# Performance work log

Hardware: AMD Instinct MI355X
Metric: run time of the kernel (lower is better)

## Reference

```python
import jax, jax.numpy as jnp
import numpy as np

N = 50000        # bs * n_node
E = 800000       # n_edge
INPUT_NF = 64
HIDDEN_NF = 64
N_CHANNEL = 4
D = 3            # spatial dim
EDGE_D = 16
EPS = 1e-12      # F.normalize clamp


def _unif(k, shape, fan_in):
    s = 1.0 / np.sqrt(fan_in)
    return jax.random.uniform(k, shape, jnp.float32, -s, s)


def setup_inputs() -> dict:
    key = jax.random.key(0)
    ks = jax.random.split(key, 12)
    h = jax.random.normal(ks[0], (N, INPUT_NF), jnp.float32)
    coord = jax.random.normal(ks[1], (N, N_CHANNEL, D), jnp.float32)
    row = jax.random.randint(ks[2], (E,), 0, N)
    col = jax.random.randint(ks[3], (E,), 0, N)
    edge_attr = jax.random.normal(ks[4], (E, EDGE_D), jnp.float32)
    kv_in = INPUT_NF + N_CHANNEL * N_CHANNEL + EDGE_D
    Wq = _unif(ks[5], (INPUT_NF, HIDDEN_NF), INPUT_NF)
    bq = _unif(ks[6], (HIDDEN_NF,), INPUT_NF)
    Wkv = _unif(ks[7], (kv_in, 2 * HIDDEN_NF), kv_in)
    bkv = _unif(ks[8], (2 * HIDDEN_NF,), kv_in)
    W1 = _unif(ks[9], (HIDDEN_NF, HIDDEN_NF), HIDDEN_NF)
    b1 = _unif(ks[10], (HIDDEN_NF,), HIDDEN_NF)
    # xavier_uniform with gain=0.001, no bias
    lim = 0.001 * np.sqrt(6.0 / (HIDDEN_NF + N_CHANNEL))
    W2 = jax.random.uniform(ks[11], (HIDDEN_NF, N_CHANNEL), jnp.float32, -lim, lim)
    return dict(h=h, coord=coord, row=row, col=col, edge_attr=edge_attr,
                Wq=Wq, bq=bq, Wkv=Wkv, bkv=bkv, W1=W1, b1=b1, W2=W2)


def reference(h, coord, edge_attr, Wq, bq, Wkv, bkv, W1, b1, W2, row, col):
    n_node = h.shape[0]
    # coord2radial
    coord_diff = coord[row] - coord[col]                                # [E,C,D]
    radial = jnp.einsum('ecd,efd->ecf', coord_diff, coord_diff)         # [E,C,C]
    # F.normalize(radial, dim=0): L2-normalize across the edge dimension
    norm = jnp.maximum(jnp.sqrt(jnp.sum(radial * radial, axis=0, keepdims=True)), EPS)
    radial = radial / norm
    # att_model
    q = h[row] @ Wq + bq                                                # [E,H]
    target_feat = jnp.concatenate(
        [radial.reshape(radial.shape[0], -1), h[col], edge_attr], axis=1)
    kv = target_feat @ Wkv + bkv                                        # [E,2H]
    k, v = kv[:, 0::2], kv[:, 1::2]                                     # [E,H] each
    alpha = jnp.sum(q * k, axis=1)                                      # [E]
    # scatter_softmax over segments given by row (numerically stable)
    seg_max = jax.ops.segment_max(alpha, row, num_segments=n_node)
    ex = jnp.exp(alpha - seg_max[row])
    seg_sum = jax.ops.segment_sum(ex, row, num_segments=n_node)
    att = ex / seg_sum[row]                                             # [E]
    # node_model (dropout in eval mode = identity)
    h_out = h + jax.ops.segment_sum(att[:, None] * v, row, num_segments=n_node)
    # coord_model: coord_mlp = Linear -> SiLU -> Linear(no bias)
    coord_v = att[:, None] * (jax.nn.silu(v @ W1 + b1) @ W2)            # [E,C]
    trans = coord_diff * coord_v[:, :, None]                            # [E,C,D]
    coord_out = coord + jax.ops.segment_sum(trans, row, num_segments=n_node)
    return h_out, coord_out, att
```

## Files before the change

kernel.cpp:

```cpp
#include <hip/hip_runtime.h>
#include <math.h>

#define NN 50000
#define NE 800000
#define NPREB 1024

typedef __attribute__((ext_vector_type(8))) short short8;
typedef __attribute__((ext_vector_type(4))) float floatx4;

__device__ __forceinline__ unsigned short bf16_of(float x) {
  unsigned u = __float_as_uint(x);
  u += 0x7fffu + ((u >> 16) & 1u);
  return (unsigned short)(u >> 16);
}
__device__ __forceinline__ float bf2f(unsigned short u) {
  return __uint_as_float(((unsigned)u) << 16);
}
__device__ __forceinline__ unsigned pack_bf(float a, float b) {
  unsigned ua = __float_as_uint(a); ua += 0x7fffu + ((ua >> 16) & 1u);
  unsigned ub = __float_as_uint(b); ub += 0x7fffu + ((ub >> 16) & 1u);
  return (ua >> 16) | (ub & 0xffff0000u);
}
__device__ __forceinline__ float blo(unsigned w) { return __uint_as_float(w << 16); }
__device__ __forceinline__ float bhi(unsigned w) { return __uint_as_float(w & 0xffff0000u); }

__global__ __launch_bounds__(256)
void k_pre(const float* __restrict__ coord, const int* __restrict__ row,
           const int* __restrict__ col, const float* __restrict__ Wkv,
           const float* __restrict__ W1, const float* __restrict__ Wq,
           float* __restrict__ norm_part, int* __restrict__ deg,
           unsigned short* __restrict__ Bkvb, unsigned short* __restrict__ W1tb,
           unsigned short* __restrict__ Wqtb) {
  __shared__ float nred[4][16];
  const int gid = blockIdx.x * 256 + threadIdx.x;
  const int np = gridDim.x * 256;
  for (int idx = gid; idx < 128 * 96; idx += np) {
    int n = idx & 127, kk = idx >> 7;
    float w = (n < 64) ? Wkv[kk * 128 + 2 * n] : Wkv[kk * 128 + 2 * (n - 64) + 1];
    Bkvb[n * 104 + kk] = bf16_of(w);
  }
  for (int idx = gid; idx < 64 * 64; idx += np) {
    int n = idx & 63, kk = idx >> 6;
    W1tb[n * 88 + kk] = bf16_of(W1[kk * 64 + n]);
  }
  for (int idx = gid; idx < 64 * 64; idx += np) {
    int n = idx & 63, kk = idx >> 6;
    Wqtb[n * 64 + kk] = bf16_of(Wq[kk * 64 + n]);
  }
  float accv[16];
#pragma unroll
  for (int j = 0; j < 16; ++j) accv[j] = 0.f;
  for (int e = gid; e < NE; e += np) {
    int r = row[e], c = col[e];
    const float4* cr = (const float4*)(coord + (size_t)r * 12);
    const float4* cc = (const float4*)(coord + (size_t)c * 12);
    float cd[12];
#pragma unroll
    for (int q = 0; q < 3; ++q) {
      float4 a = cr[q], b = cc[q];
      cd[q * 4 + 0] = a.x - b.x; cd[q * 4 + 1] = a.y - b.y;
      cd[q * 4 + 2] = a.z - b.z; cd[q * 4 + 3] = a.w - b.w;
    }
#pragma unroll
    for (int c4 = 0; c4 < 4; ++c4)
#pragma unroll
      for (int f4 = 0; f4 < 4; ++f4) {
        float v = cd[c4 * 3] * cd[f4 * 3] + cd[c4 * 3 + 1] * cd[f4 * 3 + 1] +
                  cd[c4 * 3 + 2] * cd[f4 * 3 + 2];
        accv[c4 * 4 + f4] += v * v;
      }
    atomicAdd(deg + r, 1);
  }
  const int lane = threadIdx.x & 63, wvb = threadIdx.x >> 6;
#pragma unroll
  for (int j = 0; j < 16; ++j) {
    accv[j] += __shfl_xor(accv[j], 1);
    accv[j] += __shfl_xor(accv[j], 2);
    accv[j] += __shfl_xor(accv[j], 4);
    accv[j] += __shfl_xor(accv[j], 8);
    accv[j] += __shfl_xor(accv[j], 16);
    accv[j] += __shfl_xor(accv[j], 32);
  }
  if (lane == 0) {
#pragma unroll
    for (int j = 0; j < 16; ++j) nred[wvb][j] = accv[j];
  }
  __syncthreads();
  if (threadIdx.x < 16) {
    float s = nred[0][threadIdx.x] + nred[1][threadIdx.x] +
              nred[2][threadIdx.x] + nred[3][threadIdx.x];
    norm_part[blockIdx.x * 16 + threadIdx.x] = s;
  }
}

__global__ __launch_bounds__(1024)
void k_scanq(const int* __restrict__ deg, int* __restrict__ cursor,
             const float* __restrict__ norm_part, float* __restrict__ rnorm,
             const float* __restrict__ h, const unsigned short* __restrict__ Wqtb,
             const float* __restrict__ bq,
             unsigned short* __restrict__ qg2, unsigned short* __restrict__ hb) {
  __shared__ int part[1024];
  __shared__ float nr[64][16];
  __shared__ __align__(16) unsigned short sH[16][16][72];
  const int t = threadIdx.x;
  if (blockIdx.x == 0) {
    {
      const int i = t >> 4, c = t & 15;
      float s = 0.f;
#pragma unroll
      for (int j = 0; j < NPREB / 64; ++j) s += norm_part[((i + 64 * j) << 4) + c];
      nr[i][c] = s;
    }
    __syncthreads();
    if (t < 16) {
      float s = 0.f;
#pragma unroll 8
      for (int i = 0; i < 64; ++i) s += nr[i][t];
      rnorm[t] = 1.0f / fmaxf(sqrtf(s), 1e-12f);
    }
    const int CH = (NN + 1023) / 1024;
    const int lo = t * CH, hi = (lo + CH < NN) ? lo + CH : NN;
    int s = 0;
    for (int i = lo; i < hi; ++i) s += deg[i];
    part[t] = s;
    __syncthreads();
    for (int off = 1; off < 1024; off <<= 1) {
      int v = (t >= off) ? part[t - off] : 0;
      __syncthreads();
      part[t] += v;
      __syncthreads();
    }
    int base = (t == 0) ? 0 : part[t - 1];
    for (int i = lo; i < hi; ++i) {
      cursor[i] = base; base += deg[i];
    }
    return;
  }
  const int wv = t >> 6, lane = t & 63;
  const int nbase = (blockIdx.x - 1) * 256 + wv * 16;
  if (nbase >= NN) return;
  const float4* hsrc = (const float4*)(h + (size_t)nbase * 64);
#pragma unroll
  for (int i = 0; i < 4; ++i) {
    int fi = i * 64 + lane;
    int nd = fi >> 4, c4 = fi & 15;
    float4 v = hsrc[fi];
    uint2 u; u.x = pack_bf(v.x, v.y); u.y = pack_bf(v.z, v.w);
    *(uint2*)&sH[wv][nd][c4 * 4] = u;
    *(uint2*)&hb[((size_t)nbase + nd) * 64 + c4 * 4] = u;
  }
  const int m16 = lane & 15, quad = lane >> 4;
  floatx4 acc[4];
#pragma unroll
  for (int i = 0; i < 4; ++i) acc[i] = (floatx4){0.f, 0.f, 0.f, 0.f};
#pragma unroll
  for (int ks = 0; ks < 2; ++ks) {
    short8 af = *(const short8*)&sH[wv][m16][ks * 32 + quad * 8];
#pragma unroll
    for (int nt = 0; nt < 4; ++nt) {
      short8 bf = *(const short8*)&Wqtb[(nt * 16 + m16) * 64 + ks * 32 + quad * 8];
      acc[nt] = __builtin_amdgcn_mfma_f32_16x16x32_bf16(af, bf, acc[nt], 0, 0, 0);
    }
  }
  const float bq0 = bq[m16], bq1 = bq[16 + m16];
  const float bq2 = bq[32 + m16], bq3 = bq[48 + m16];
#pragma unroll
  for (int r = 0; r < 4; ++r) {
    size_t nd = (size_t)nbase + quad * 4 + r;
    uint2 u;
    u.x = pack_bf(acc[0][r] + bq0, acc[1][r] + bq1);
    u.y = pack_bf(acc[2][r] + bq2, acc[3][r] + bq3);
    *(uint2*)&qg2[nd * 64 + m16 * 4] = u;
  }
}

__global__ void k_scatter(const int* __restrict__ row, const int* __restrict__ col,
                          const float* __restrict__ edge_attr,
                          int* __restrict__ cursor, int* __restrict__ iperm,
                          unsigned* __restrict__ rcp, uint4* __restrict__ eab) {
  int e = blockIdx.x * 256 + threadIdx.x;
  if (e < NE) {
    int r = row[e], c = col[e];
    int p = atomicAdd(cursor + r, 1);
    iperm[e] = p;
    rcp[p] = ((unsigned)r << 16) | (unsigned)c;
    const float4* ep = (const float4*)(edge_attr + (size_t)e * 16);
    float4 f0 = ep[0], f1 = ep[1], f2 = ep[2], f3 = ep[3];
    uint4 a, b;
    a.x = pack_bf(f0.x, f0.y); a.y = pack_bf(f0.z, f0.w);
    a.z = pack_bf(f1.x, f1.y); a.w = pack_bf(f1.z, f1.w);
    b.x = pack_bf(f2.x, f2.y); b.y = pack_bf(f2.z, f2.w);
    b.z = pack_bf(f3.x, f3.y); b.w = pack_bf(f3.z, f3.w);
    eab[(size_t)p * 2]     = a;
    eab[(size_t)p * 2 + 1] = b;
  }
}

__global__ __launch_bounds__(512, 6)
void k_kv(const unsigned short* __restrict__ hb, const float* __restrict__ coord,
          const float* __restrict__ bkv, const float* __restrict__ b1,
          const float* __restrict__ W2, const float* __restrict__ rnorm,
          const unsigned* __restrict__ rcp, const uint4* __restrict__ eab,
          const unsigned short* __restrict__ Bkvb,
          const unsigned short* __restrict__ W1tb,
          const unsigned short* __restrict__ qg2,
          float* __restrict__ exg, float* __restrict__ l_g,
          float* __restrict__ hacc_g, float* __restrict__ cacc_g) {
  __shared__ __align__(16) unsigned short sA[128][104];
  __shared__ __align__(16) unsigned short sB[128][104];
  __shared__ unsigned sRC[128];
  unsigned short (*sW1t)[88] = (unsigned short (*)[88])&sB[0][0];

  const int tid = threadIdx.x;
  const int base = blockIdx.x * 128;

  const uint4* gw = (const uint4*)W1tb;
  uint4 w1a = gw[tid];
  uint4 w1b;
  if (tid < 192) w1b = gw[512 + tid];

  if (tid < 128) sRC[tid] = rcp[base + tid];
  if (tid < 256) {
    int s = tid >> 1;
    *(uint4*)&sA[s][80 + (tid & 1) * 8] = eab[(size_t)base * 2 + tid];
  }
  for (int idx = tid; idx < 1024; idx += 512) {
    int s = idx >> 3, k8 = idx & 7;
    unsigned c = rcp[base + s] & 0xffffu;
    uint4 u = ((const uint4*)(hb + (size_t)c * 64))[k8];
    *(uint4*)&sA[s][16 + k8 * 8] = u;
  }
  {
    const uint4* gb = (const uint4*)Bkvb;
    uint4* sb = (uint4*)&sB[0][0];
    for (int idx = tid; idx < 1664; idx += 512) sb[idx] = gb[idx];
  }
  const int wv = tid >> 6, lane = tid & 63;
  float cdp[4];
  {
    const int grp = lane >> 4, g = lane & 15;
    const int c4 = g >> 2, f4 = g & 3;
    const float rn = rnorm[g];
#pragma unroll
    for (int it = 0; it < 4; ++it) {
      int slot = 16 * wv + it * 4 + grp;
      unsigned rc = rcp[base + slot];
      int r = (int)(rc >> 16), c = (int)(rc & 0xffffu);
      float cd = 0.f;
      if (g < 12) cd = coord[r * 12 + g] - coord[c * 12 + g];
      cdp[it] = cd;
      float rad = 0.f;
#pragma unroll
      for (int d = 0; d < 3; ++d)
        rad += __shfl(cd, grp * 16 + c4 * 3 + d) * __shfl(cd, grp * 16 + f4 * 3 + d);
      sA[slot][g] = bf16_of(rad * rn);
    }
  }
  __syncthreads();

  const int m16 = lane & 15, quad = lane >> 4;
  const int arow = 16 * wv + m16;

  floatx4 acc[8];
#pragma unroll
  for (int i = 0; i < 8; ++i) acc[i] = (floatx4){0.f, 0.f, 0.f, 0.f};
#pragma unroll
  for (int ks = 0; ks < 3; ++ks) {
    short8 af = *(const short8*)&sA[arow][ks * 32 + quad * 8];
#pragma unroll
    for (int nt = 0; nt < 8; ++nt) {
      short8 bf = *(const short8*)&sB[nt * 16 + m16][ks * 32 + quad * 8];
      acc[nt] = __builtin_amdgcn_mfma_f32_16x16x32_bf16(af, bf, acc[nt], 0, 0, 0);
    }
  }
#pragma unroll
  for (int nt = 0; nt < 4; ++nt) {
    float bk = bkv[2 * (m16 + 16 * nt)];
    float bv = bkv[2 * (m16 + 16 * nt) + 1];
#pragma unroll
    for (int r = 0; r < 4; ++r) { acc[nt][r] += bk; acc[nt + 4][r] += bv; }
  }
  float part[4] = {0.f, 0.f, 0.f, 0.f};
#pragma unroll
  for (int r = 0; r < 4; ++r) {
    unsigned nrow = sRC[16 * wv + quad * 4 + r] >> 16;
    uint2 qp = *(const uint2*)(qg2 + (size_t)nrow * 64 + m16 * 4);
    part[r] += blo(qp.x) * acc[0][r] + bhi(qp.x) * acc[1][r] +
               blo(qp.y) * acc[2][r] + bhi(qp.y) * acc[3][r];
  }
#pragma unroll
  for (int off = 1; off < 16; off <<= 1) {
#pragma unroll
    for (int r = 0; r < 4; ++r) part[r] += __shfl_xor(part[r], off);
  }
  float ex[4];
#pragma unroll
  for (int r = 0; r < 4; ++r) ex[r] = __expf(part[r]);
  if (m16 == 0) {
#pragma unroll
    for (int r = 0; r < 4; ++r)
      exg[base + 16 * wv + quad * 4 + r] = ex[r];
  }
#pragma unroll
  for (int nt = 0; nt < 4; ++nt)
#pragma unroll
    for (int r = 0; r < 4; ++r)
      sA[16 * wv + quad * 4 + r][m16 + 16 * nt] = bf16_of(acc[4 + nt][r]);
#pragma unroll
  for (int it = 0; it < 4; ++it)
    if (m16 < 12) sA[16 * wv + it * 4 + quad][64 + m16] = bf16_of(cdp[it]);

  __syncthreads();
  {
    unsigned short* sw = &sB[0][0];
    *(uint4*)&sw[(size_t)tid * 8] = w1a;
    if (tid < 192) *(uint4*)&sw[(size_t)(512 + tid) * 8] = w1b;
  }
  __syncthreads();

  floatx4 tacc[4];
#pragma unroll
  for (int i = 0; i < 4; ++i) tacc[i] = (floatx4){0.f, 0.f, 0.f, 0.f};
#pragma unroll
  for (int ks = 0; ks < 2; ++ks) {
    short8 af = *(const short8*)&sA[arow][ks * 32 + quad * 8];
#pragma unroll
    for (int nt = 0; nt < 4; ++nt) {
      short8 bf = *(const short8*)&sW1t[nt * 16 + m16][ks * 32 + quad * 8];
      tacc[nt] = __builtin_amdgcn_mfma_f32_16x16x32_bf16(af, bf, tacc[nt], 0, 0, 0);
    }
  }
#pragma unroll
  for (int nt = 0; nt < 4; ++nt) {
    float bb = b1[m16 + 16 * nt];
#pragma unroll
    for (int r = 0; r < 4; ++r) {
      float t = tacc[nt][r] + bb;
      tacc[nt][r] = t * __builtin_amdgcn_rcpf(1.f + __expf(-t));
    }
  }
  float w0[16];
#pragma unroll
  for (int r = 0; r < 4; ++r)
#pragma unroll
    for (int c = 0; c < 4; ++c) w0[r * 4 + c] = 0.f;
#pragma unroll
  for (int nt = 0; nt < 4; ++nt) {
    float4 w2r = ((const float4*)W2)[m16 + 16 * nt];
#pragma unroll
    for (int r = 0; r < 4; ++r) {
      w0[r * 4 + 0] += tacc[nt][r] * w2r.x;
      w0[r * 4 + 1] += tacc[nt][r] * w2r.y;
      w0[r * 4 + 2] += tacc[nt][r] * w2r.z;
      w0[r * 4 + 3] += tacc[nt][r] * w2r.w;
    }
  }
  float rs1[8];
#pragma unroll
  for (int jj = 0; jj < 8; ++jj) {
    float snd = (m16 & 8) ? w0[jj] : w0[jj + 8];
    float rcv = __shfl_xor(snd, 8);
    rs1[jj] = ((m16 & 8) ? w0[jj + 8] : w0[jj]) + rcv;
  }
  float rs2[4];
#pragma unroll
  for (int jj = 0; jj < 4; ++jj) {
    float snd = (m16 & 4) ? rs1[jj] : rs1[jj + 4];
    float rcv = __shfl_xor(snd, 4);
    rs2[jj] = ((m16 & 4) ? rs1[jj + 4] : rs1[jj]) + rcv;
  }
  float rs3[2];
#pragma unroll
  for (int jj = 0; jj < 2; ++jj) {
    float snd = (m16 & 2) ? rs2[jj] : rs2[jj + 2];
    float rcv = __shfl_xor(snd, 2);
    rs3[jj] = ((m16 & 2) ? rs2[jj + 2] : rs2[jj]) + rcv;
  }
  float cvtot;
  {
    float snd = (m16 & 1) ? rs3[0] : rs3[1];
    float rcv = __shfl_xor(snd, 1);
    cvtot = ((m16 & 1) ? rs3[1] : rs3[0]) + rcv;
  }
  const int d3 = (m16 < 12) ? ((m16 * 11) >> 5) : 3;
  float tr[4];
#pragma unroll
  for (int r = 0; r < 4; ++r) {
    float cvv = __shfl(cvtot, (quad << 4) + r * 4 + d3);
    tr[r] = (m16 < 12) ? bf2f(sA[16 * wv + quad * 4 + r][64 + m16]) * cvv : 0.f;
  }

  int s = 0;
  while (s < 16) {
    int n = (int)(sRC[16 * wv + s] >> 16);
    int e2 = s + 1;
    while (e2 < 16 && (int)(sRC[16 * wv + e2] >> 16) == n) ++e2;
    float hp0 = 0.f, hp1 = 0.f, hp2 = 0.f, hp3 = 0.f, lp = 0.f, cp = 0.f;
#pragma unroll
    for (int r = 0; r < 4; ++r) {
      int rowi = quad * 4 + r;
      float w = (rowi >= s && rowi < e2) ? ex[r] : 0.f;
      hp0 += w * acc[4][r];
      hp1 += w * acc[5][r];
      hp2 += w * acc[6][r];
      hp3 += w * acc[7][r];
      lp  += (rowi >= s && rowi < e2) ? ex[r] : 0.f;
      cp  += w * tr[r];
    }
    hp0 += __shfl_xor(hp0, 16); hp0 += __shfl_xor(hp0, 32);
    hp1 += __shfl_xor(hp1, 16); hp1 += __shfl_xor(hp1, 32);
    hp2 += __shfl_xor(hp2, 16); hp2 += __shfl_xor(hp2, 32);
    hp3 += __shfl_xor(hp3, 16); hp3 += __shfl_xor(hp3, 32);
    lp  += __shfl_xor(lp, 16);  lp  += __shfl_xor(lp, 32);
    cp  += __shfl_xor(cp, 16);  cp  += __shfl_xor(cp, 32);
    if (quad == 0) {
      float* hg = hacc_g + (size_t)n * 64;
      atomicAdd(hg + m16,      hp0);
      atomicAdd(hg + m16 + 16, hp1);
      atomicAdd(hg + m16 + 32, hp2);
      atomicAdd(hg + m16 + 48, hp3);
      if (m16 < 12) atomicAdd(cacc_g + (size_t)n * 12 + m16, cp);
      if (m16 == 0) atomicAdd(l_g + n, lp);
    }
    s = e2;
  }
}

__global__ __launch_bounds__(256)
void k_fin(const float* __restrict__ h, const float* __restrict__ coord,
           const int* __restrict__ row, const int* __restrict__ iperm,
           const float* __restrict__ exg, const float* __restrict__ l_g,
           const float* __restrict__ hacc_g, const float* __restrict__ cacc_g,
           float* __restrict__ out) {
  const int node = blockIdx.x * 16 + (threadIdx.x >> 4);
  const int q16 = threadIdx.x & 15;
  const float l = l_g[node];
  const float inv = (l > 0.f) ? 1.f / l : 0.f;
  {
    float4 hv = ((const float4*)(h + (size_t)node * 64))[q16];
    float4 av = ((const float4*)(hacc_g + (size_t)node * 64))[q16];
    float4 o;
    o.x = hv.x + av.x * inv; o.y = hv.y + av.y * inv;
    o.z = hv.z + av.z * inv; o.w = hv.w + av.w * inv;
    ((float4*)(out + (size_t)node * 64))[q16] = o;
  }
  if (q16 < 3) {
    float4 cv = ((const float4*)(coord + (size_t)node * 12))[q16];
    float4 av = ((const float4*)(cacc_g + (size_t)node * 12))[q16];
    float4 o;
    o.x = cv.x + av.x * inv; o.y = cv.y + av.y * inv;
    o.z = cv.z + av.z * inv; o.w = cv.w + av.w * inv;
    ((float4*)(out + (size_t)NN * 64 + (size_t)node * 12))[q16] = o;
  }
  const int e = blockIdx.x * 256 + threadIdx.x;
  float le = l_g[row[e]];
  out[(size_t)NN * 64 + NN * 12 + e] = exg[iperm[e]] * __builtin_amdgcn_rcpf(le);
}

extern "C" void kernel_launch(void* const* d_in, const int* in_sizes, int n_in,
                              void* d_out, int out_size, void* d_ws, size_t ws_size,
                              hipStream_t stream) {
  const float* h         = (const float*)d_in[0];
  const float* coord     = (const float*)d_in[1];
  const int*   row       = (const int*)d_in[2];
  const int*   col       = (const int*)d_in[3];
  const float* edge_attr = (const float*)d_in[4];
  const float* Wq        = (const float*)d_in[5];
  const float* bq        = (const float*)d_in[6];
  const float* Wkv       = (const float*)d_in[7];
  const float* bkv       = (const float*)d_in[8];
  const float* W1        = (const float*)d_in[9];
  const float* b1        = (const float*)d_in[10];
  const float* W2        = (const float*)d_in[11];
  float* out = (float*)d_out;

  size_t off = 0;
  char* wsb = (char*)d_ws;
  auto alloc = [&](size_t bytes) {
    off = (off + 255) & ~(size_t)255;
    void* p = wsb + off; off += bytes; return p;
  };
  int*            deg      = (int*)alloc((size_t)NN * 4);
  float*          l_g      = (float*)alloc((size_t)NN * 4);
  float*          hacc_g   = (float*)alloc((size_t)NN * 64 * 4);
  float*          cacc_g   = (float*)alloc((size_t)NN * 12 * 4);
  size_t zbytes = off;
  float*          norm_part= (float*)alloc((size_t)NPREB * 16 * 4);
  float*          rnorm    = (float*)alloc(16 * 4);
  int*            cursor   = (int*)alloc((size_t)NN * 4);
  unsigned*       rcp      = (unsigned*)alloc((size_t)NE * 4);
  int*            iperm    = (int*)alloc((size_t)NE * 4);
  float*          exg      = (float*)alloc((size_t)NE * 4);
  uint4*          eab      = (uint4*)alloc((size_t)NE * 32);
  unsigned short* qg2      = (unsigned short*)alloc((size_t)NN * 64 * 2);
  unsigned short* hb       = (unsigned short*)alloc((size_t)NN * 64 * 2);
  unsigned short* Bkvb     = (unsigned short*)alloc(128 * 104 * 2);
  unsigned short* W1tb     = (unsigned short*)alloc(64 * 88 * 2);
  unsigned short* Wqtb     = (unsigned short*)alloc(64 * 64 * 2);

  hipMemsetAsync(d_ws, 0, zbytes, stream);

  k_pre<<<NPREB, 256, 0, stream>>>(coord, row, col, Wkv, W1, Wq,
                                   norm_part, deg, Bkvb, W1tb, Wqtb);
  k_scanq<<<1 + (NN + 255) / 256, 1024, 0, stream>>>(deg, cursor, norm_part,
                                                     rnorm, h, Wqtb, bq, qg2, hb);
  k_scatter<<<(NE + 255) / 256, 256, 0, stream>>>(row, col, edge_attr, cursor,
                                                  iperm, rcp, eab);
  k_kv<<<NE / 128, 512, 0, stream>>>(hb, coord, bkv, b1, W2, rnorm,
                                     rcp, eab, Bkvb, W1tb, qg2,
                                     exg, l_g, hacc_g, cacc_g);
  k_fin<<<NN / 16, 256, 0, stream>>>(h, coord, row, iperm, exg, l_g,
                                     hacc_g, cacc_g, out);
}
```

Baseline: 429.9 us.

## Move radial norm reduction into scatter pass and fuse degree count with q projection

The edge-wise coord-diff radial norm accumulation moves from the pre-pass into the scatter kernel, which already reads row/col per edge, so the coordinate gathers piggyback on an existing pass. The degree histogram is merged with the h->bf16 conversion and q projection in one kernel that stages Wq in shared memory, and the scan and norm finalisation become small separate single-block kernels. This removes a full edge pass over row/col and coord gathers, at the cost of one extra kernel launch and a larger norm partial array.

```diff
diff --git a/kernel.cpp b/kernel.cpp
--- a/kernel.cpp
+++ b/kernel.cpp
@@ -3,7 +3,7 @@
 
 #define NN 50000
 #define NE 800000
-#define NPREB 1024
+#define NSCB 3136
 
 typedef __attribute__((ext_vector_type(8))) short short8;
 typedef __attribute__((ext_vector_type(4))) float floatx4;
@@ -24,16 +24,22 @@
 __device__ __forceinline__ float blo(unsigned w) { return __uint_as_float(w << 16); }
 __device__ __forceinline__ float bhi(unsigned w) { return __uint_as_float(w & 0xffff0000u); }
 
-__global__ __launch_bounds__(256)
-void k_pre(const float* __restrict__ coord, const int* __restrict__ row,
-           const int* __restrict__ col, const float* __restrict__ Wkv,
-           const float* __restrict__ W1, const float* __restrict__ Wq,
-           float* __restrict__ norm_part, int* __restrict__ deg,
-           unsigned short* __restrict__ Bkvb, unsigned short* __restrict__ W1tb,
-           unsigned short* __restrict__ Wqtb) {
-  __shared__ float nred[4][16];
-  const int gid = blockIdx.x * 256 + threadIdx.x;
-  const int np = gridDim.x * 256;
+__global__ __launch_bounds__(1024)
+void k_pre2(const int* __restrict__ row, const float* __restrict__ Wkv,
+            const float* __restrict__ W1, const float* __restrict__ Wq,
+            const float* __restrict__ bq, const float* __restrict__ h,
+            int* __restrict__ deg,
+            unsigned short* __restrict__ Bkvb, unsigned short* __restrict__ W1tb,
+            unsigned short* __restrict__ qg2, unsigned short* __restrict__ hb) {
+  __shared__ __align__(16) unsigned short sH[16][16][72];
+  __shared__ __align__(16) unsigned short sWqt[64 * 72];
+  const int t = threadIdx.x;
+  const int gid = blockIdx.x * 1024 + t;
+  const int np = gridDim.x * 1024;
+  for (int idx = t; idx < 64 * 64; idx += 1024) {
+    int n = idx & 63, kk = idx >> 6;
+    sWqt[n * 72 + kk] = bf16_of(Wq[kk * 64 + n]);
+  }
   for (int idx = gid; idx < 128 * 96; idx += np) {
     int n = idx & 127, kk = idx >> 7;
     float w = (n < 64) ? Wkv[kk * 128 + 2 * n] : Wkv[kk * 128 + 2 * (n - 64) + 1];
@@ -43,101 +49,11 @@
     int n = idx & 63, kk = idx >> 6;
     W1tb[n * 88 + kk] = bf16_of(W1[kk * 64 + n]);
   }
-  for (int idx = gid; idx < 64 * 64; idx += np) {
-    int n = idx & 63, kk = idx >> 6;
-    Wqtb[n * 64 + kk] = bf16_of(Wq[kk * 64 + n]);
-  }
-  float accv[16];
-#pragma unroll
-  for (int j = 0; j < 16; ++j) accv[j] = 0.f;
-  for (int e = gid; e < NE; e += np) {
-    int r = row[e], c = col[e];
-    const float4* cr = (const float4*)(coord + (size_t)r * 12);
-    const float4* cc = (const float4*)(coord + (size_t)c * 12);
-    float cd[12];
-#pragma unroll
-    for (int q = 0; q < 3; ++q) {
-      float4 a = cr[q], b = cc[q];
-      cd[q * 4 + 0] = a.x - b.x; cd[q * 4 + 1] = a.y - b.y;
-      cd[q * 4 + 2] = a.z - b.z; cd[q * 4 + 3] = a.w - b.w;
-    }
-#pragma unroll
-    for (int c4 = 0; c4 < 4; ++c4)
-#pragma unroll
-      for (int f4 = 0; f4 < 4; ++f4) {
-        float v = cd[c4 * 3] * cd[f4 * 3] + cd[c4 * 3 + 1] * cd[f4 * 3 + 1] +
-                  cd[c4 * 3 + 2] * cd[f4 * 3 + 2];
-        accv[c4 * 4 + f4] += v * v;
-      }
-    atomicAdd(deg + r, 1);
-  }
-  const int lane = threadIdx.x & 63, wvb = threadIdx.x >> 6;
-#pragma unroll
-  for (int j = 0; j < 16; ++j) {
-    accv[j] += __shfl_xor(accv[j], 1);
-    accv[j] += __shfl_xor(accv[j], 2);
-    accv[j] += __shfl_xor(accv[j], 4);
-    accv[j] += __shfl_xor(accv[j], 8);
-    accv[j] += __shfl_xor(accv[j], 16);
-    accv[j] += __shfl_xor(accv[j], 32);
-  }
-  if (lane == 0) {
-#pragma unroll
-    for (int j = 0; j < 16; ++j) nred[wvb][j] = accv[j];
-  }
-  __syncthreads();
-  if (threadIdx.x < 16) {
-    float s = nred[0][threadIdx.x] + nred[1][threadIdx.x] +
-              nred[2][threadIdx.x] + nred[3][threadIdx.x];
-    norm_part[blockIdx.x * 16 + threadIdx.x] = s;
-  }
-}
-
-__global__ __launch_bounds__(1024)
-void k_scanq(const int* __restrict__ deg, int* __restrict__ cursor,
-             const float* __restrict__ norm_part, float* __restrict__ rnorm,
-             const float* __restrict__ h, const unsigned short* __restrict__ Wqtb,
-             const float* __restrict__ bq,
-             unsigned short* __restrict__ qg2, unsigned short* __restrict__ hb) {
-  __shared__ int part[1024];
-  __shared__ float nr[64][16];
-  __shared__ __align__(16) unsigned short sH[16][16][72];
-  const int t = threadIdx.x;
-  if (blockIdx.x == 0) {
-    {
-      const int i = t >> 4, c = t & 15;
-      float s = 0.f;
-#pragma unroll
-      for (int j = 0; j < NPREB / 64; ++j) s += norm_part[((i + 64 * j) << 4) + c];
-      nr[i][c] = s;
-    }
-    __syncthreads();
-    if (t < 16) {
-      float s = 0.f;
-#pragma unroll 8
-      for (int i = 0; i < 64; ++i) s += nr[i][t];
-      rnorm[t] = 1.0f / fmaxf(sqrtf(s), 1e-12f);
-    }
-    const int CH = (NN + 1023) / 1024;
-    const int lo = t * CH, hi = (lo + CH < NN) ? lo + CH : NN;
-    int s = 0;
-    for (int i = lo; i < hi; ++i) s += deg[i];
-    part[t] = s;
-    __syncthreads();
-    for (int off = 1; off < 1024; off <<= 1) {
-      int v = (t >= off) ? part[t - off] : 0;
-      __syncthreads();
-      part[t] += v;
-      __syncthreads();
-    }
-    int base = (t == 0) ? 0 : part[t - 1];
-    for (int i = lo; i < hi; ++i) {
-      cursor[i] = base; base += deg[i];
-    }
-    return;
-  }
+  for (int e = gid; e < NE; e += np) atomicAdd(deg + row[e], 1);
+  __syncthreads();
   const int wv = t >> 6, lane = t & 63;
-  const int nbase = (blockIdx.x - 1) * 256 + wv * 16;
+  const int tile = blockIdx.x * 16 + wv;
+  const int nbase = tile * 16;
   if (nbase >= NN) return;
   const float4* hsrc = (const float4*)(h + (size_t)nbase * 64);
 #pragma unroll
@@ -158,7 +74,7 @@
     short8 af = *(const short8*)&sH[wv][m16][ks * 32 + quad * 8];
 #pragma unroll
     for (int nt = 0; nt < 4; ++nt) {
-      short8 bf = *(const short8*)&Wqtb[(nt * 16 + m16) * 64 + ks * 32 + quad * 8];
+      short8 bf = *(const short8*)&sWqt[(nt * 16 + m16) * 72 + ks * 32 + quad * 8];
       acc[nt] = __builtin_amdgcn_mfma_f32_16x16x32_bf16(af, bf, acc[nt], 0, 0, 0);
     }
   }
@@ -174,11 +90,39 @@
   }
 }
 
-__global__ void k_scatter(const int* __restrict__ row, const int* __restrict__ col,
-                          const float* __restrict__ edge_attr,
-                          int* __restrict__ cursor, int* __restrict__ iperm,
-                          unsigned* __restrict__ rcp, uint4* __restrict__ eab) {
-  int e = blockIdx.x * 256 + threadIdx.x;
+__global__ __launch_bounds__(1024)
+void k_scan(const int* __restrict__ deg, int* __restrict__ cursor) {
+  __shared__ int part[1024];
+  const int t = threadIdx.x;
+  const int CH = (NN + 1023) / 1024;
+  const int lo = t * CH, hi = (lo + CH < NN) ? lo + CH : NN;
+  int s = 0;
+  for (int i = lo; i < hi; ++i) s += deg[i];
+  part[t] = s;
+  __syncthreads();
+  for (int off = 1; off < 1024; off <<= 1) {
+    int v = (t >= off) ? part[t - off] : 0;
+    __syncthreads();
+    part[t] += v;
+    __syncthreads();
+  }
+  int base = (t == 0) ? 0 : part[t - 1];
+  for (int i = lo; i < hi; ++i) {
+    cursor[i] = base; base += deg[i];
+  }
+}
+
+__global__ __launch_bounds__(256)
+void k_scatter(const int* __restrict__ row, const int* __restrict__ col,
+               const float* __restrict__ edge_attr, const float* __restrict__ coord,
+               int* __restrict__ cursor, int* __restrict__ iperm,
+               unsigned* __restrict__ rcp, uint4* __restrict__ eab,
+               float* __restrict__ norm_part) {
+  __shared__ float nred[4][16];
+  const int e = blockIdx.x * 256 + threadIdx.x;
+  float accv[16];
+#pragma unroll
+  for (int j = 0; j < 16; ++j) accv[j] = 0.f;
   if (e < NE) {
     int r = row[e], c = col[e];
     int p = atomicAdd(cursor + r, 1);
@@ -193,6 +137,60 @@
     b.z = pack_bf(f3.x, f3.y); b.w = pack_bf(f3.z, f3.w);
     eab[(size_t)p * 2]     = a;
     eab[(size_t)p * 2 + 1] = b;
+    const float4* cr = (const float4*)(coord + (size_t)r * 12);
+    const float4* cc = (const float4*)(coord + (size_t)c * 12);
+    float cd[12];
+#pragma unroll
+    for (int q = 0; q < 3; ++q) {
+      float4 av = cr[q], bv = cc[q];
+      cd[q * 4 + 0] = av.x - bv.x; cd[q * 4 + 1] = av.y - bv.y;
+      cd[q * 4 + 2] = av.z - bv.z; cd[q * 4 + 3] = av.w - bv.w;
+    }
+#pragma unroll
+    for (int c4 = 0; c4 < 4; ++c4)
+#pragma unroll
+      for (int f4 = 0; f4 < 4; ++f4) {
+        float v = cd[c4 * 3] * cd[f4 * 3] + cd[c4 * 3 + 1] * cd[f4 * 3 + 1] +
+                  cd[c4 * 3 + 2] * cd[f4 * 3 + 2];
+        accv[c4 * 4 + f4] += v * v;
+      }
+  }
+  const int lane = threadIdx.x & 63, wvb = threadIdx.x >> 6;
+#pragma unroll
+  for (int j = 0; j < 16; ++j) {
+    accv[j] += __shfl_xor(accv[j], 1);
+    accv[j] += __shfl_xor(accv[j], 2);
+    accv[j] += __shfl_xor(accv[j], 4);
+    accv[j] += __shfl_xor(accv[j], 8);
+    accv[j] += __shfl_xor(accv[j], 16);
+    accv[j] += __shfl_xor(accv[j], 32);
+  }
+  if (lane == 0) {
+#pragma unroll
+    for (int j = 0; j < 16; ++j) nred[wvb][j] = accv[j];
+  }
+  __syncthreads();
+  if (threadIdx.x < 16) {
+    float s = nred[0][threadIdx.x] + nred[1][threadIdx.x] +
+              nred[2][threadIdx.x] + nred[3][threadIdx.x];
+    norm_part[blockIdx.x * 16 + threadIdx.x] = s;
+  }
+}
+
+__global__ __launch_bounds__(256)
+void k_rnorm(const float* __restrict__ norm_part, float* __restrict__ rnorm) {
+  __shared__ float nr[16][16];
+  const int t = threadIdx.x;
+  const int i = t >> 4, c = t & 15;
+  float s = 0.f;
+  for (int j = 0; j < NSCB / 16; ++j) s += norm_part[((i + 16 * j) << 4) + c];
+  nr[i][c] = s;
+  __syncthreads();
+  if (t < 16) {
+    float s2 = 0.f;
+#pragma unroll
+    for (int k = 0; k < 16; ++k) s2 += nr[k][t];
+    rnorm[t] = 1.0f / fmaxf(sqrtf(s2), 1e-12f);
   }
 }
 
@@ -485,7 +483,7 @@
   float*          hacc_g   = (float*)alloc((size_t)NN * 64 * 4);
   float*          cacc_g   = (float*)alloc((size_t)NN * 12 * 4);
   size_t zbytes = off;
-  float*          norm_part= (float*)alloc((size_t)NPREB * 16 * 4);
+  float*          norm_part= (float*)alloc((size_t)NSCB * 16 * 4);
   float*          rnorm    = (float*)alloc(16 * 4);
   int*            cursor   = (int*)alloc((size_t)NN * 4);
   unsigned*       rcp      = (unsigned*)alloc((size_t)NE * 4);
@@ -496,16 +494,15 @@
   unsigned short* hb       = (unsigned short*)alloc((size_t)NN * 64 * 2);
   unsigned short* Bkvb     = (unsigned short*)alloc(128 * 104 * 2);
   unsigned short* W1tb     = (unsigned short*)alloc(64 * 88 * 2);
-  unsigned short* Wqtb     = (unsigned short*)alloc(64 * 64 * 2);
 
   hipMemsetAsync(d_ws, 0, zbytes, stream);
 
-  k_pre<<<NPREB, 256, 0, stream>>>(coord, row, col, Wkv, W1, Wq,
-                                   norm_part, deg, Bkvb, W1tb, Wqtb);
-  k_scanq<<<1 + (NN + 255) / 256, 1024, 0, stream>>>(deg, cursor, norm_part,
-                                                     rnorm, h, Wqtb, bq, qg2, hb);
-  k_scatter<<<(NE + 255) / 256, 256, 0, stream>>>(row, col, edge_attr, cursor,
-                                                  iperm, rcp, eab);
+  k_pre2<<<196, 1024, 0, stream>>>(row, Wkv, W1, Wq, bq, h,
+                                   deg, Bkvb, W1tb, qg2, hb);
+  k_scan<<<1, 1024, 0, stream>>>(deg, cursor);
+  k_scatter<<<NSCB, 256, 0, stream>>>(row, col, edge_attr, coord,
+                                      cursor, iperm, rcp, eab, norm_part);
+  k_rnorm<<<1, 256, 0, stream>>>(norm_part, rnorm);
   k_kv<<<NE / 128, 512, 0, stream>>>(hb, coord, bkv, b1, W2, rnorm,
                                      rcp, eab, Bkvb, W1tb, qg2,
                                      exg, l_g, hacc_g, cacc_g);
```

Result: slower. 458.4 us (+6.6%).
